# Performance work log

Hardware: AMD Instinct MI355X
Metric: run time of the kernel (lower is better)

## Reference

```python
import jax, jax.numpy as jnp
import numpy as np

UNITS = 256
EPS = 0.01
GAMMA = 0.01
BETA = 0.8
ALPHA = 1.0


def setup_inputs() -> dict:
    key = jax.random.key(0)
    k1, k2, k3, k4 = jax.random.split(key, 4)
    x = jax.random.normal(k1, (64, 2048, 256), dtype=jnp.float32)
    C = jax.random.normal(k2, (UNITS, UNITS), dtype=jnp.float32) * 0.05
    B = jax.random.normal(k3, (UNITS, UNITS), dtype=jnp.float32) * 0.05
    U = jax.random.normal(k4, (256, UNITS), dtype=jnp.float32) * 0.05
    b = jnp.zeros((UNITS,), dtype=jnp.float32)
    return {"x": x, "C": C, "B": B, "U": U, "b": b}


def reference(x, C, B, U, b):
    # Loop-invariant matrices (skew/symmetric mix minus gamma*I), built once.
    I = jnp.eye(UNITS, dtype=x.dtype)
    A = BETA * (B - B.T) + (1.0 - BETA) * (B + B.T) - GAMMA * I
    W = BETA * (C - C.T) + (1.0 - BETA) * (C + C.T) - GAMMA * I

    # Precompute input projection for all timesteps: [batch, T, units]
    xu = jnp.einsum('bti,iu->btu', x, U) + b
    xu_t = jnp.swapaxes(xu, 0, 1)  # [T, batch, units] for scan

    h0 = jnp.zeros((x.shape[0], UNITS), dtype=x.dtype)

    def step(h, xu_step):
        h_new = h + EPS * ALPHA * (h @ A) + EPS * jnp.tanh(h @ W + xu_step)
        return h_new, h_new

    _, hs = jax.lax.scan(step, h0, xu_t)  # hs: [T, batch, units]
    return jnp.swapaxes(hs, 0, 1)  # [batch, T, units]
```

## Files before the change

kernel.cpp:

```cpp
#include <hip/hip_runtime.h>

#define EPS 0.01f
#define TSTEPS 2048
#define BATCH 64
#define TWOLOG2E 2.8853900817779268f

typedef _Float16 half8 __attribute__((ext_vector_type(8)));
typedef _Float16 half4 __attribute__((ext_vector_type(4)));
typedef float f32x4 __attribute__((ext_vector_type(4)));

#define LDS_BARRIER() asm volatile("s_waitcnt lgkmcnt(0)\n\ts_barrier" ::: "memory")

__global__ void prep_mc_pack(const float* __restrict__ Bm, const float* __restrict__ Cm,
                             _Float16* __restrict__ mcPack) {
    int f = blockIdx.x;
    int lane = threadIdx.x;
    int w = f >> 4;
    int mt = (f >> 3) & 1;
    int kk = f & 7;
    const float* Src = (mt == 0) ? Bm : Cm;
    float scale = (mt == 0) ? 1.0f : TWOLOG2E;
    int c = 16 * w + (lane & 15);
    int k0 = kk * 32 + (lane >> 4) * 8;
    long off = ((long)f * 64 + lane) * 8;
#pragma unroll
    for (int j = 0; j < 8; ++j) {
        int k = k0 + j;
        float diag = (k == c) ? 0.01f : 0.0f;
        float v = scale * (Src[(long)k * 256 + c] - 0.6f * Src[(long)c * 256 + k] - diag);
        mcPack[off + j] = (_Float16)v;
    }
}

__global__ void pack_u(const float* __restrict__ U, _Float16* __restrict__ up) {
    int t = blockIdx.x * 64 + threadIdx.x;
    int lane = t & 63;
    int tile = t >> 6;
    int nn = tile & 15;
    int kk = tile >> 4;
    int krow = kk * 32 + (lane >> 4) * 8;
    int col = nn * 16 + (lane & 15);
    long off = (long)t * 8;
#pragma unroll
    for (int jj = 0; jj < 8; ++jj) {
        up[off + jj] = (_Float16)U[(krow + jj) * 256 + col];
    }
}

__global__ __launch_bounds__(256) void xu_gemm(const float* __restrict__ x,
                                               const _Float16* __restrict__ up,
                                               const float* __restrict__ bias,
                                               float* __restrict__ out) {
    int wave = threadIdx.x >> 6;
    int lane = threadIdx.x & 63;
    int m = lane & 15;
    int quad = lane >> 4;
    long row0 = (long)blockIdx.x * 64 + wave * 16;
    const float* xrow = x + (row0 + m) * 256 + quad * 8;

    f32x4 acc[16];
#pragma unroll
    for (int nn = 0; nn < 16; ++nn) acc[nn] = (f32x4){0.f, 0.f, 0.f, 0.f};

#pragma unroll
    for (int kk = 0; kk < 8; ++kk) {
        f32x4 xa = *(const f32x4*)(xrow + kk * 32);
        f32x4 xb = *(const f32x4*)(xrow + kk * 32 + 4);
        half8 af;
        af[0] = (_Float16)xa[0]; af[1] = (_Float16)xa[1];
        af[2] = (_Float16)xa[2]; af[3] = (_Float16)xa[3];
        af[4] = (_Float16)xb[0]; af[5] = (_Float16)xb[1];
        af[6] = (_Float16)xb[2]; af[7] = (_Float16)xb[3];
        const _Float16* ub = up + ((long)kk * 1024 + lane) * 8;
#pragma unroll
        for (int nn = 0; nn < 16; ++nn) {
            half8 bf = *(const half8*)(ub + (long)nn * 512);
            acc[nn] = __builtin_amdgcn_mfma_f32_16x16x32_f16(af, bf, acc[nn], 0, 0, 0);
        }
    }
#pragma unroll
    for (int nn = 0; nn < 16; ++nn) {
        int col = nn * 16 + m;
        float bv = bias[col];
#pragma unroll
        for (int i = 0; i < 4; ++i) {
            out[(row0 + quad * 4 + i) * 256 + col] = (acc[nn][i] + bv) * TWOLOG2E;
        }
    }
}

__global__ __launch_bounds__(1024, 4) void scan_kernel(const _Float16* __restrict__ mcPack,
                                                       float* __restrict__ io) {
    const int tid = threadIdx.x;
    const int w = tid >> 6;
    const int lane = tid & 63;
    const int m = lane & 15;
    const int q = lane >> 4;
    const int b0 = blockIdx.x * 16;

    half8 mcf[2][8];
#pragma unroll
    for (int mt = 0; mt < 2; ++mt)
#pragma unroll
        for (int kk = 0; kk < 8; ++kk)
            mcf[mt][kk] = *(const half8*)(mcPack + (((long)(w * 2 + mt) * 8 + kk) * 64 + lane) * 8);

    __shared__ _Float16 hB[2][4096];

    {
        half4 z = (half4)(_Float16)0.0f;
        *(half4*)(&hB[0][tid * 4]) = z;
    }

    const int rdIdx = lane * 8;
    const int wrIdx = 512 * (w >> 1) + 256 * (w & 1) + 128 * (q >> 1) + 8 * m + 4 * (q & 1);

    float* p = io + ((long)(b0 + m) * TSTEPS) * 256 + 16 * w + 4 * q;

    f32x4 hs = (f32x4){0.f, 0.f, 0.f, 0.f};

    f32x4 xq[2];
    xq[0] = *(const f32x4*)(p);
    xq[1] = *(const f32x4*)(p + 256);
    __syncthreads();

    auto step = [&](int t, const _Float16* hbR, _Float16* hbW, f32x4& xc) {
        half8 hb0 = *(const half8*)(hbR + 0 * 512 + rdIdx);
        half8 hb1 = *(const half8*)(hbR + 1 * 512 + rdIdx);
        half8 hb2 = *(const half8*)(hbR + 2 * 512 + rdIdx);
        half8 hb3 = *(const half8*)(hbR + 3 * 512 + rdIdx);

        f32x4 aA = __builtin_amdgcn_mfma_f32_16x16x32_f16(mcf[0][0], hb0, hs, 0, 0, 0);
        f32x4 aW = __builtin_amdgcn_mfma_f32_16x16x32_f16(mcf[1][0], hb0, xc, 0, 0, 0);
        aA = __builtin_amdgcn_mfma_f32_16x16x32_f16(mcf[0][1], hb1, aA, 0, 0, 0);
        aW = __builtin_amdgcn_mfma_f32_16x16x32_f16(mcf[1][1], hb1, aW, 0, 0, 0);
        aA = __builtin_amdgcn_mfma_f32_16x16x32_f16(mcf[0][2], hb2, aA, 0, 0, 0);
        aW = __builtin_amdgcn_mfma_f32_16x16x32_f16(mcf[1][2], hb2, aW, 0, 0, 0);
        aA = __builtin_amdgcn_mfma_f32_16x16x32_f16(mcf[0][3], hb3, aA, 0, 0, 0);
        aW = __builtin_amdgcn_mfma_f32_16x16x32_f16(mcf[1][3], hb3, aW, 0, 0, 0);

        half8 hb4 = *(const half8*)(hbR + 4 * 512 + rdIdx);
        half8 hb5 = *(const half8*)(hbR + 5 * 512 + rdIdx);
        half8 hb6 = *(const half8*)(hbR + 6 * 512 + rdIdx);
        half8 hb7 = *(const half8*)(hbR + 7 * 512 + rdIdx);

        aA = __builtin_amdgcn_mfma_f32_16x16x32_f16(mcf[0][4], hb4, aA, 0, 0, 0);
        aW = __builtin_amdgcn_mfma_f32_16x16x32_f16(mcf[1][4], hb4, aW, 0, 0, 0);
        aA = __builtin_amdgcn_mfma_f32_16x16x32_f16(mcf[0][5], hb5, aA, 0, 0, 0);
        aW = __builtin_amdgcn_mfma_f32_16x16x32_f16(mcf[1][5], hb5, aW, 0, 0, 0);
        aA = __builtin_amdgcn_mfma_f32_16x16x32_f16(mcf[0][6], hb6, aA, 0, 0, 0);
        aW = __builtin_amdgcn_mfma_f32_16x16x32_f16(mcf[1][6], hb6, aW, 0, 0, 0);
        aA = __builtin_amdgcn_mfma_f32_16x16x32_f16(mcf[0][7], hb7, aA, 0, 0, 0);
        aW = __builtin_amdgcn_mfma_f32_16x16x32_f16(mcf[1][7], hb7, aW, 0, 0, 0);

        f32x4 hn;
#pragma unroll
        for (int i = 0; i < 4; ++i) {
            float e = __builtin_amdgcn_exp2f(aW[i]);
            float r = __builtin_amdgcn_rcpf(e + 1.0f);
            float hsv = fmaf(-2.0f, r, aA[i] + 1.0f);
            hs[i] = hsv;
            hn[i] = EPS * hsv;
        }
        half4 h4;
#pragma unroll
        for (int i = 0; i < 4; ++i) h4[i] = (_Float16)hn[i];
        *(half4*)(hbW + wrIdx) = h4;
        *(f32x4*)(p) = hn;

        if (t + 2 < TSTEPS) {
            xc = *(const f32x4*)(p + 512);
        }
        p += 256;
        LDS_BARRIER();
    };

    for (int t = 0; t < TSTEPS; t += 2) {
        step(t, hB[0], hB[1], xq[0]);
        step(t + 1, hB[1], hB[0], xq[1]);
    }
}

extern "C" void kernel_launch(void* const* d_in, const int* in_sizes, int n_in,
                              void* d_out, int out_size, void* d_ws, size_t ws_size,
                              hipStream_t stream) {
    const float* x    = (const float*)d_in[0];
    const float* C    = (const float*)d_in[1];
    const float* Bm   = (const float*)d_in[2];
    const float* U    = (const float*)d_in[3];
    const float* bias = (const float*)d_in[4];
    float* out = (float*)d_out;

    _Float16* mcPack = (_Float16*)d_ws;
    _Float16* up     = (_Float16*)((char*)d_ws + 262144);

    prep_mc_pack<<<256, 64, 0, stream>>>(Bm, C, mcPack);
    pack_u<<<128, 64, 0, stream>>>(U, up);
    xu_gemm<<<2048, 256, 0, stream>>>(x, up, bias, out);
    scan_kernel<<<4, 1024, 0, stream>>>(mcPack, out);
}
```

Baseline: 2.233 ms.

## Split each batch group's recurrence across two workgroups with global-memory handoff

The scan kernel now runs 8 workgroups of 512 threads instead of 4 of 1024. Each pair of workgroups shares one 16-row batch group and each computes half of the 256 hidden units. Every step, each workgroup writes its half of h to a global staging buffer, publishes a step flag, and spins on its partner's flag before reading the remote half. The aim is to halve per-workgroup MFMA and barrier cost and spread the work over more CUs, at the price of a cross-CU global-memory round trip and a spin-wait on the serial critical path every timestep.

```diff
diff --git a/kernel.cpp b/kernel.cpp
--- a/kernel.cpp
+++ b/kernel.cpp
@@ -8,19 +8,19 @@
 typedef _Float16 half8 __attribute__((ext_vector_type(8)));
 typedef _Float16 half4 __attribute__((ext_vector_type(4)));
 typedef float f32x4 __attribute__((ext_vector_type(4)));
-
-#define LDS_BARRIER() asm volatile("s_waitcnt lgkmcnt(0)\n\ts_barrier" ::: "memory")
+typedef unsigned long long u64;
+typedef u64 u64x2 __attribute__((ext_vector_type(2)));
 
 __global__ void prep_mc_pack(const float* __restrict__ Bm, const float* __restrict__ Cm,
                              _Float16* __restrict__ mcPack) {
     int f = blockIdx.x;
     int lane = threadIdx.x;
-    int w = f >> 4;
+    int G = f >> 4;
     int mt = (f >> 3) & 1;
     int kk = f & 7;
     const float* Src = (mt == 0) ? Bm : Cm;
     float scale = (mt == 0) ? 1.0f : TWOLOG2E;
-    int c = 16 * w + (lane & 15);
+    int c = 16 * G + (lane & 15);
     int k0 = kk * 32 + (lane >> 4) * 8;
     long off = ((long)f * 64 + lane) * 8;
 #pragma unroll
@@ -45,6 +45,12 @@
     for (int jj = 0; jj < 8; ++jj) {
         up[off + jj] = (_Float16)U[(krow + jj) * 256 + col];
     }
+}
+
+__global__ void zero_sync(u64* __restrict__ stg, int* __restrict__ flags) {
+    int t = blockIdx.x * 256 + threadIdx.x;
+    stg[t] = 0ull;
+    if (t < 128) flags[t] = 0;
 }
 
 __global__ __launch_bounds__(256) void xu_gemm(const float* __restrict__ x,
@@ -89,23 +95,33 @@
     }
 }
 
-__global__ __launch_bounds__(1024, 4) void scan_kernel(const _Float16* __restrict__ mcPack,
-                                                       float* __restrict__ io) {
+__global__ __launch_bounds__(512, 2) void scan_kernel(const _Float16* __restrict__ mcPack,
+                                                      float* __restrict__ io,
+                                                      u64* __restrict__ stg,
+                                                      int* __restrict__ flags) {
     const int tid = threadIdx.x;
     const int w = tid >> 6;
     const int lane = tid & 63;
     const int m = lane & 15;
     const int q = lane >> 4;
-    const int b0 = blockIdx.x * 16;
+    const int b = blockIdx.x;
+    const int g = b >> 1;
+    const int u = b & 1;
+    const int G = 8 * u + w;
+
+    const int KL = 4 * u;
+    const int KR = 4 - KL;
 
     half8 mcf[2][8];
 #pragma unroll
     for (int mt = 0; mt < 2; ++mt)
 #pragma unroll
-        for (int kk = 0; kk < 8; ++kk)
-            mcf[mt][kk] = *(const half8*)(mcPack + (((long)(w * 2 + mt) * 8 + kk) * 64 + lane) * 8);
-
-    __shared__ _Float16 hB[2][4096];
+        for (int j = 0; j < 8; ++j) {
+            int kk = (j < 4) ? (KL + j) : (KR + j - 4);
+            mcf[mt][j] = *(const half8*)(mcPack + (((long)(G * 2 + mt) * 8 + kk) * 64 + lane) * 8);
+        }
+
+    __shared__ _Float16 hB[2][2048];
 
     {
         half4 z = (half4)(_Float16)0.0f;
@@ -115,7 +131,14 @@
     const int rdIdx = lane * 8;
     const int wrIdx = 512 * (w >> 1) + 256 * (w & 1) + 128 * (q >> 1) + 8 * m + 4 * (q & 1);
 
-    float* p = io + ((long)(b0 + m) * TSTEPS) * 256 + 16 * w + 4 * q;
+    u64* const stgOwn0 = stg + ((long)b * 2 + 0) * 512;
+    u64* const stgOwn1 = stg + ((long)b * 2 + 1) * 512;
+    u64* const stgRem0 = stg + ((long)(b ^ 1) * 2 + 0) * 512;
+    u64* const stgRem1 = stg + ((long)(b ^ 1) * 2 + 1) * 512;
+    int* const flagOwn = flags + b * 16;
+    int* const flagRem = flags + (b ^ 1) * 16;
+
+    float* p = io + ((long)(16 * g + m) * TSTEPS) * 256 + 128 * u + 16 * w + 4 * q;
 
     f32x4 hs = (f32x4){0.f, 0.f, 0.f, 0.f};
 
@@ -124,34 +147,47 @@
     xq[1] = *(const f32x4*)(p + 256);
     __syncthreads();
 
-    auto step = [&](int t, const _Float16* hbR, _Float16* hbW, f32x4& xc) {
-        half8 hb0 = *(const half8*)(hbR + 0 * 512 + rdIdx);
-        half8 hb1 = *(const half8*)(hbR + 1 * 512 + rdIdx);
-        half8 hb2 = *(const half8*)(hbR + 2 * 512 + rdIdx);
-        half8 hb3 = *(const half8*)(hbR + 3 * 512 + rdIdx);
-
-        f32x4 aA = __builtin_amdgcn_mfma_f32_16x16x32_f16(mcf[0][0], hb0, hs, 0, 0, 0);
-        f32x4 aW = __builtin_amdgcn_mfma_f32_16x16x32_f16(mcf[1][0], hb0, xc, 0, 0, 0);
-        aA = __builtin_amdgcn_mfma_f32_16x16x32_f16(mcf[0][1], hb1, aA, 0, 0, 0);
-        aW = __builtin_amdgcn_mfma_f32_16x16x32_f16(mcf[1][1], hb1, aW, 0, 0, 0);
-        aA = __builtin_amdgcn_mfma_f32_16x16x32_f16(mcf[0][2], hb2, aA, 0, 0, 0);
-        aW = __builtin_amdgcn_mfma_f32_16x16x32_f16(mcf[1][2], hb2, aW, 0, 0, 0);
-        aA = __builtin_amdgcn_mfma_f32_16x16x32_f16(mcf[0][3], hb3, aA, 0, 0, 0);
-        aW = __builtin_amdgcn_mfma_f32_16x16x32_f16(mcf[1][3], hb3, aW, 0, 0, 0);
-
-        half8 hb4 = *(const half8*)(hbR + 4 * 512 + rdIdx);
-        half8 hb5 = *(const half8*)(hbR + 5 * 512 + rdIdx);
-        half8 hb6 = *(const half8*)(hbR + 6 * 512 + rdIdx);
-        half8 hb7 = *(const half8*)(hbR + 7 * 512 + rdIdx);
-
-        aA = __builtin_amdgcn_mfma_f32_16x16x32_f16(mcf[0][4], hb4, aA, 0, 0, 0);
-        aW = __builtin_amdgcn_mfma_f32_16x16x32_f16(mcf[1][4], hb4, aW, 0, 0, 0);
-        aA = __builtin_amdgcn_mfma_f32_16x16x32_f16(mcf[0][5], hb5, aA, 0, 0, 0);
-        aW = __builtin_amdgcn_mfma_f32_16x16x32_f16(mcf[1][5], hb5, aW, 0, 0, 0);
-        aA = __builtin_amdgcn_mfma_f32_16x16x32_f16(mcf[0][6], hb6, aA, 0, 0, 0);
-        aW = __builtin_amdgcn_mfma_f32_16x16x32_f16(mcf[1][6], hb6, aW, 0, 0, 0);
-        aA = __builtin_amdgcn_mfma_f32_16x16x32_f16(mcf[0][7], hb7, aA, 0, 0, 0);
-        aW = __builtin_amdgcn_mfma_f32_16x16x32_f16(mcf[1][7], hb7, aW, 0, 0, 0);
+    auto step = [&](int t, const _Float16* hbR, _Float16* hbW,
+                    u64* remIn, u64* ownOut, f32x4& xc) {
+        while (__hip_atomic_load(flagRem, __ATOMIC_RELAXED, __HIP_MEMORY_SCOPE_AGENT) < t) {}
+        asm volatile("" ::: "memory");
+
+        u64 rl0 = __hip_atomic_load(remIn + 0 * 128 + lane * 2,     __ATOMIC_RELAXED, __HIP_MEMORY_SCOPE_AGENT);
+        u64 rh0 = __hip_atomic_load(remIn + 0 * 128 + lane * 2 + 1, __ATOMIC_RELAXED, __HIP_MEMORY_SCOPE_AGENT);
+        u64 rl1 = __hip_atomic_load(remIn + 1 * 128 + lane * 2,     __ATOMIC_RELAXED, __HIP_MEMORY_SCOPE_AGENT);
+        u64 rh1 = __hip_atomic_load(remIn + 1 * 128 + lane * 2 + 1, __ATOMIC_RELAXED, __HIP_MEMORY_SCOPE_AGENT);
+        u64 rl2 = __hip_atomic_load(remIn + 2 * 128 + lane * 2,     __ATOMIC_RELAXED, __HIP_MEMORY_SCOPE_AGENT);
+        u64 rh2 = __hip_atomic_load(remIn + 2 * 128 + lane * 2 + 1, __ATOMIC_RELAXED, __HIP_MEMORY_SCOPE_AGENT);
+        u64 rl3 = __hip_atomic_load(remIn + 3 * 128 + lane * 2,     __ATOMIC_RELAXED, __HIP_MEMORY_SCOPE_AGENT);
+        u64 rh3 = __hip_atomic_load(remIn + 3 * 128 + lane * 2 + 1, __ATOMIC_RELAXED, __HIP_MEMORY_SCOPE_AGENT);
+
+        half8 l0 = *(const half8*)(hbR + 0 * 512 + rdIdx);
+        half8 l1 = *(const half8*)(hbR + 1 * 512 + rdIdx);
+        half8 l2 = *(const half8*)(hbR + 2 * 512 + rdIdx);
+        half8 l3 = *(const half8*)(hbR + 3 * 512 + rdIdx);
+
+        f32x4 aA = __builtin_amdgcn_mfma_f32_16x16x32_f16(mcf[0][0], l0, hs, 0, 0, 0);
+        f32x4 aW = __builtin_amdgcn_mfma_f32_16x16x32_f16(mcf[1][0], l0, xc, 0, 0, 0);
+        aA = __builtin_amdgcn_mfma_f32_16x16x32_f16(mcf[0][1], l1, aA, 0, 0, 0);
+        aW = __builtin_amdgcn_mfma_f32_16x16x32_f16(mcf[1][1], l1, aW, 0, 0, 0);
+        aA = __builtin_amdgcn_mfma_f32_16x16x32_f16(mcf[0][2], l2, aA, 0, 0, 0);
+        aW = __builtin_amdgcn_mfma_f32_16x16x32_f16(mcf[1][2], l2, aW, 0, 0, 0);
+        aA = __builtin_amdgcn_mfma_f32_16x16x32_f16(mcf[0][3], l3, aA, 0, 0, 0);
+        aW = __builtin_amdgcn_mfma_f32_16x16x32_f16(mcf[1][3], l3, aW, 0, 0, 0);
+
+        half8 r0 = __builtin_bit_cast(half8, (u64x2){rl0, rh0});
+        half8 r1 = __builtin_bit_cast(half8, (u64x2){rl1, rh1});
+        half8 r2 = __builtin_bit_cast(half8, (u64x2){rl2, rh2});
+        half8 r3 = __builtin_bit_cast(half8, (u64x2){rl3, rh3});
+
+        aA = __builtin_amdgcn_mfma_f32_16x16x32_f16(mcf[0][4], r0, aA, 0, 0, 0);
+        aW = __builtin_amdgcn_mfma_f32_16x16x32_f16(mcf[1][4], r0, aW, 0, 0, 0);
+        aA = __builtin_amdgcn_mfma_f32_16x16x32_f16(mcf[0][5], r1, aA, 0, 0, 0);
+        aW = __builtin_amdgcn_mfma_f32_16x16x32_f16(mcf[1][5], r1, aW, 0, 0, 0);
+        aA = __builtin_amdgcn_mfma_f32_16x16x32_f16(mcf[0][6], r2, aA, 0, 0, 0);
+        aW = __builtin_amdgcn_mfma_f32_16x16x32_f16(mcf[1][6], r2, aW, 0, 0, 0);
+        aA = __builtin_amdgcn_mfma_f32_16x16x32_f16(mcf[0][7], r3, aA, 0, 0, 0);
+        aW = __builtin_amdgcn_mfma_f32_16x16x32_f16(mcf[1][7], r3, aW, 0, 0, 0);
 
         f32x4 hn;
 #pragma unroll
@@ -165,19 +201,25 @@
         half4 h4;
 #pragma unroll
         for (int i = 0; i < 4; ++i) h4[i] = (_Float16)hn[i];
+
         *(half4*)(hbW + wrIdx) = h4;
+        __hip_atomic_store(ownOut + (wrIdx >> 2), __builtin_bit_cast(u64, h4),
+                           __ATOMIC_RELAXED, __HIP_MEMORY_SCOPE_AGENT);
+
+        asm volatile("s_waitcnt vmcnt(0) lgkmcnt(0)\n\ts_barrier" ::: "memory");
+        if (tid == 0)
+            __hip_atomic_store(flagOwn, t + 1, __ATOMIC_RELAXED, __HIP_MEMORY_SCOPE_AGENT);
+
         *(f32x4*)(p) = hn;
-
         if (t + 2 < TSTEPS) {
             xc = *(const f32x4*)(p + 512);
         }
         p += 256;
-        LDS_BARRIER();
     };
 
     for (int t = 0; t < TSTEPS; t += 2) {
-        step(t, hB[0], hB[1], xq[0]);
-        step(t + 1, hB[1], hB[0], xq[1]);
+        step(t,     hB[0], hB[1], stgRem0, stgOwn1, xq[0]);
+        step(t + 1, hB[1], hB[0], stgRem1, stgOwn0, xq[1]);
     }
 }
 
@@ -193,9 +235,12 @@
 
     _Float16* mcPack = (_Float16*)d_ws;
     _Float16* up     = (_Float16*)((char*)d_ws + 262144);
+    u64*      stg    = (u64*)((char*)d_ws + 393216);
+    int*      flags  = (int*)((char*)d_ws + 458752);
 
     prep_mc_pack<<<256, 64, 0, stream>>>(Bm, C, mcPack);
     pack_u<<<128, 64, 0, stream>>>(U, up);
+    zero_sync<<<32, 256, 0, stream>>>(stg, flags);
     xu_gemm<<<2048, 256, 0, stream>>>(x, up, bias, out);
-    scan_kernel<<<4, 1024, 0, stream>>>(mcPack, out);
-}
+    scan_kernel<<<8, 512, 0, stream>>>(mcPack, out, stg, flags);
+}
```

Measured after the change: 4.286 ms. 91.9% more time.
